# Optimization experiments

Hardware: AMD Instinct MI355X
Metric: run time of the kernel (lower is better)

Reference implementation:

```python
import math
import jax, jax.numpy as jnp
import numpy as np

B, N, D, H = 8, 512, 1024, 16
HD = D // H
K_DEFAULT, K_MAX, PROX_THR = 8, 12, 20.0


def setup_inputs() -> dict:
    key = jax.random.key(0)
    ks = jax.random.split(key, 12)
    tokens_B = jax.random.normal(ks[0], (B, N, D), dtype=jnp.float32)
    ego_distances = jax.random.uniform(ks[1], (B, N), dtype=jnp.float32)
    ego_mask = jnp.zeros((B, N), dtype=bool).at[:, 0].set(True)  # token 0 is ego
    ego_speed = jax.random.uniform(ks[2], (B,), dtype=jnp.float32)
    s = 1.0 / math.sqrt(D)
    Wq = jax.random.normal(ks[3], (D, D), jnp.float32) * s
    Wk = jax.random.normal(ks[4], (D, D), jnp.float32) * s
    Wv = jax.random.normal(ks[5], (D, D), jnp.float32) * s
    Weq = jax.random.normal(ks[6], (D, D), jnp.float32) * s
    Wo = jax.random.normal(ks[7], (D, D), jnp.float32) * (0.02 * s)
    Dm = D // 4
    W1 = jax.random.normal(ks[8], (Dm, 2), jnp.float32) * (1.0 / math.sqrt(2))
    b1 = jnp.zeros((Dm,), jnp.float32)
    W2 = jax.random.normal(ks[9], (H, Dm), jnp.float32) * (1.0 / math.sqrt(Dm))
    b2 = jnp.zeros((H,), jnp.float32)
    return dict(tokens_B=tokens_B, ego_distances=ego_distances, ego_mask=ego_mask,
                ego_speed=ego_speed, Wq=Wq, Wk=Wk, Wv=Wv, Weq=Weq, Wo=Wo,
                W1=W1, b1=b1, W2=W2, b2=b2)


def _compute_K(ego_speed, ego_distances):
    # deterministic, no-grad lookup (torch: @torch.no_grad)
    n = ego_distances.shape[1]
    close = (ego_distances < PROX_THR).astype(jnp.float32).sum(-1)
    density = close / max(n, 1)
    avg_speed = float(jnp.mean(ego_speed))
    avg_density = float(jnp.mean(density))
    K = K_DEFAULT
    if avg_speed > 15.0:
        K = min(K + 1, K_MAX)
    if avg_density > 0.5:
        K = min(K + 1, K_MAX)
    return min(K, n - 1)


def reference(tokens_B, ego_distances, ego_mask, ego_speed, Wq, Wk, Wv, Weq, Wo, W1, b1, W2, b2):
    b, n, d = tokens_B.shape
    K = _compute_K(ego_speed, ego_distances)
    if K <= 0:
        return jnp.zeros_like(tokens_B)

    # top-K nearest-to-ego neighbors per token, excluding self
    eye = jnp.eye(n, dtype=bool)
    dist_rank = jnp.where(eye[None, :, :], jnp.inf, ego_distances[:, None, :])  # (B,N,N)
    _, topk_idx = jax.lax.top_k(-dist_rank, K)  # (B,N,K) indices of smallest dists

    neighbors = jax.vmap(lambda t, idx: t[idx])(tokens_B, topk_idx)  # (B,N,K,D)

    is_ego = ego_mask.astype(tokens_B.dtype)[..., None]
    Q = (1.0 - is_ego) * (tokens_B @ Wq.T) + is_ego * (tokens_B @ Weq.T)
    Km = neighbors @ Wk.T
    Vm = neighbors @ Wv.T

    Q = Q.reshape(b, n, H, HD).transpose(0, 2, 1, 3)              # (B,H,N,hd)
    Km = Km.reshape(b, n, K, H, HD).transpose(0, 3, 1, 2, 4)      # (B,H,N,K,hd)
    Vm = Vm.reshape(b, n, K, H, HD).transpose(0, 3, 1, 2, 4)

    scores = jnp.einsum('bhnd,bhnkd->bhnk', Q, Km) / math.sqrt(HD)

    # additive pairwise distance bias MLP on (d_i_to_ego, d_j_to_ego)
    d_i = jnp.broadcast_to(ego_distances[:, :, None], (b, n, K))
    d_j = jax.vmap(lambda dd, idx: dd[idx])(ego_distances, topk_idx)
    dist_pair = jnp.stack([d_i, d_j], axis=-1)                    # (B,N,K,2)
    bias = jax.nn.relu(dist_pair @ W1.T + b1) @ W2.T + b2         # (B,N,K,H)
    scores = scores + bias.transpose(0, 3, 1, 2)                  # FIX-1: additive

    attn = jax.nn.softmax(scores, axis=-1)
    out = jnp.einsum('bhnk,bhnkd->bhnd', attn, Vm)
    out = out.transpose(0, 2, 1, 3).reshape(b, n, d)              # FIX-2 axis order
    return out @ Wo.T
```

## Files before the change

kernel.cpp:

```cpp
#include <hip/hip_runtime.h>
#include <math.h>

#define Bn 8
#define Nn 512
#define Dn 1024
#define Hn 16
#define HDn 64
#define KMAX 12
#define NSMAX 13
#define PROX 20.0f

typedef __attribute__((ext_vector_type(8))) short bf16x8;
typedef __attribute__((ext_vector_type(4))) float f32x4;

__device__ __forceinline__ unsigned short f2bf(float f) {
    unsigned int u = __float_as_uint(f);
    return (unsigned short)((u + 0x7FFFu + ((u >> 16) & 1u)) >> 16);
}

__global__ __launch_bounds__(256) void cvt_meta_kernel(const float* __restrict__ tokens,
                                                       const float* __restrict__ Wq,
                                                       const float* __restrict__ Wo,
                                                       const float* __restrict__ Wk,
                                                       const float* __restrict__ Wv,
                                                       const float* __restrict__ dist,
                                                       const float* __restrict__ speed,
                                                       unsigned short* __restrict__ tok_h,
                                                       unsigned short* __restrict__ wq_h,
                                                       unsigned short* __restrict__ wo_h,
                                                       unsigned short* __restrict__ wkv_h,
                                                       int* __restrict__ meta,
                                                       int* __restrict__ Lidx,
                                                       unsigned short* __restrict__ tok_g) {
    int blk = blockIdx.x;
    if (blk < 8192) {
        const float* src;
        unsigned short* dst;
        int local;
        if (blk < 4096) { src = tokens; dst = tok_h; local = blk; }
        else if (blk < 5120) { src = Wq; dst = wq_h; local = blk - 4096; }
        else if (blk < 6144) { src = Wo; dst = wo_h; local = blk - 5120; }
        else if (blk < 7168) { src = Wk; dst = wkv_h; local = blk - 6144; }
        else { src = Wv; dst = wkv_h + (size_t)Dn * Dn; local = blk - 7168; }
        int i = (local * 256 + threadIdx.x) * 4;
        float4 v = *(const float4*)&src[i];
        ushort4 o;
        o.x = f2bf(v.x); o.y = f2bf(v.y); o.z = f2bf(v.z); o.w = f2bf(v.w);
        *(ushort4*)&dst[i] = o;
        return;
    }
    if (threadIdx.x >= 64) return;
    int lane = threadIdx.x;
    int b = blk - 8192;

    int cnt = 0;
    for (int i = lane; i < Bn * Nn; i += 64) cnt += (dist[i] < PROX) ? 1 : 0;
    for (int off = 32; off; off >>= 1) cnt += __shfl_xor(cnt, off);

    float sp = 0.f;
    for (int i = lane; i < Bn; i += 64) sp += speed[i];
    for (int off = 32; off; off >>= 1) sp += __shfl_xor(sp, off);

    float avg_density = (float)cnt / (float)(Bn * Nn);
    float avg_speed = sp / (float)Bn;
    int K = 8;
    if (avg_speed > 15.0f) K = min(K + 1, KMAX);
    if (avg_density > 0.5f) K = min(K + 1, KMAX);
    K = min(K, Nn - 1);
    if (b == 0 && lane == 0) meta[0] = K;
    int ns = K + 1;

    int sel[NSMAX];
    float dloc[Nn / 64];
    #pragma unroll
    for (int j = 0; j < Nn / 64; ++j) dloc[j] = dist[b * Nn + lane + 64 * j];
    for (int r = 0; r < ns; ++r) {
        float mv = 1e30f;
        int mi = 0;
        #pragma unroll
        for (int j = 0; j < Nn / 64; ++j) {
            if (dloc[j] < mv) { mv = dloc[j]; mi = lane + 64 * j; }
        }
        for (int off = 32; off; off >>= 1) {
            float ov = __shfl_xor(mv, off);
            int oi = __shfl_xor(mi, off);
            if (ov < mv || (ov == mv && oi < mi)) { mv = ov; mi = oi; }
        }
        sel[r] = mi;
        if (lane == 0) Lidx[b * NSMAX + r] = mi;
        if ((mi & 63) == lane) dloc[mi >> 6] = 1e30f;
    }

    for (int s = 0; s < ns; ++s) {
        const float* src = &tokens[(size_t)(b * Nn + sel[s]) * Dn];
        unsigned short* dst = &tok_g[(size_t)(b * NSMAX + s) * Dn];
        #pragma unroll
        for (int q = 0; q < 4; ++q) {
            float4 v = *(const float4*)&src[(q * 64 + lane) * 4];
            ushort4 o;
            o.x = f2bf(v.x); o.y = f2bf(v.y); o.z = f2bf(v.z); o.w = f2bf(v.w);
            *(ushort4*)&dst[(q * 64 + lane) * 4] = o;
        }
    }
}

__device__ __forceinline__ void gemm_body(const unsigned short* __restrict__ A,
                                          const unsigned short* __restrict__ Bm,
                                          float* __restrict__ C, int Nd,
                                          int bm, int bn,
                                          unsigned short* As, unsigned short* Bs) {
    const int Kd = Dn;
    int t = threadIdx.x;
    int wave = t >> 6, lane = t & 63;
    int wm = wave >> 1, wn = wave & 1;

    int srow = lane >> 2;
    int skoff = (lane & 3) * 8;
    const unsigned short* Ag  = A  + (size_t)(bm + wave * 16 + srow) * Kd + skoff;
    const unsigned short* Bg  = Bm + (size_t)(bn + wave * 32 + srow) * Kd + skoff;
    const unsigned short* Bg2 = Bg + 16 * Kd;
    unsigned short* AsW  = As + (wave * 16) * 32;
    unsigned short* BsW  = Bs + (wave * 32) * 32;
    unsigned short* BsW2 = BsW + 16 * 32;

    f32x4 acc[2][4] = {};

    int fm = lane & 15;
    int fk = (lane >> 4) * 8;

    for (int k0 = 0; k0 < Kd; k0 += 32) {
        __builtin_amdgcn_global_load_lds((const __attribute__((address_space(1))) void*)Ag,
                                         (__attribute__((address_space(3))) void*)AsW, 16, 0, 0);
        __builtin_amdgcn_global_load_lds((const __attribute__((address_space(1))) void*)Bg,
                                         (__attribute__((address_space(3))) void*)BsW, 16, 0, 0);
        __builtin_amdgcn_global_load_lds((const __attribute__((address_space(1))) void*)Bg2,
                                         (__attribute__((address_space(3))) void*)BsW2, 16, 0, 0);
        Ag += 32; Bg += 32; Bg2 += 32;
        __syncthreads();

        bf16x8 af[2], bfr[4];
        #pragma unroll
        for (int mi = 0; mi < 2; ++mi)
            af[mi] = *(const bf16x8*)&As[(wm * 32 + mi * 16 + fm) * 32 + fk];
        #pragma unroll
        for (int ni = 0; ni < 4; ++ni)
            bfr[ni] = *(const bf16x8*)&Bs[(wn * 64 + ni * 16 + fm) * 32 + fk];
        #pragma unroll
        for (int mi = 0; mi < 2; ++mi)
            #pragma unroll
            for (int ni = 0; ni < 4; ++ni)
                acc[mi][ni] = __builtin_amdgcn_mfma_f32_16x16x32_bf16(af[mi], bfr[ni], acc[mi][ni], 0, 0, 0);
        __syncthreads();
    }

    int erow = (lane >> 4) * 4;
    #pragma unroll
    for (int mi = 0; mi < 2; ++mi)
        #pragma unroll
        for (int ni = 0; ni < 4; ++ni)
            #pragma unroll
            for (int r = 0; r < 4; ++r) {
                int row = bm + wm * 32 + mi * 16 + erow + r;
                int col = bn + wn * 64 + ni * 16 + fm;
                C[(size_t)row * Nd + col] = acc[mi][ni][r];
            }
}

__global__ __launch_bounds__(256) void proj_fused_kernel(const unsigned short* __restrict__ tok_h,
                                                         const unsigned short* __restrict__ wq_h,
                                                         const unsigned short* __restrict__ tok_g,
                                                         const unsigned short* __restrict__ wkv_h,
                                                         const float* __restrict__ tokens,
                                                         const float* __restrict__ Weq,
                                                         float* __restrict__ Qbuf,
                                                         float* __restrict__ KVproj,
                                                         float* __restrict__ Qego) {
    __shared__ unsigned short As[64 * 32];
    __shared__ unsigned short Bs[128 * 32];
    __shared__ float tok[Dn];

    int blk = blockIdx.x;
    if (blk < 32) {
        gemm_body(tok_g, wkv_h, KVproj, 2048, (blk >> 4) * 64, (blk & 15) * 128, As, Bs);
    } else if (blk < 544) {
        int idx = blk - 32;
        gemm_body(tok_h, wq_h, Qbuf, Dn, (idx >> 3) * 64, (idx & 7) * 128, As, Bs);
    } else {
        int blk2 = blk - 544;
        int b = blk2 >> 5, cg = blk2 & 31;
        for (int t = threadIdx.x; t < Dn; t += 256) tok[t] = tokens[(size_t)(b * Nn) * Dn + t];
        __syncthreads();
        int w = threadIdx.x >> 6, lane = threadIdx.x & 63;
        for (int o = 0; o < 8; ++o) {
            int col = cg * 32 + w * 8 + o;
            const float* wr = &Weq[(size_t)col * Dn];
            float sum = 0.f;
            #pragma unroll
            for (int q = 0; q < 4; ++q) {
                float4 w4 = *(const float4*)&wr[q * 256 + lane * 4];
                float4 t4 = *(const float4*)&tok[q * 256 + lane * 4];
                sum += w4.x * t4.x + w4.y * t4.y + w4.z * t4.z + w4.w * t4.w;
            }
            for (int off = 32; off; off >>= 1) sum += __shfl_xor(sum, off);
            if (lane == 0) Qego[(size_t)b * Dn + col] = sum;
        }
    }
}

__global__ __launch_bounds__(256) void gemm_out_kernel(const unsigned short* __restrict__ A,
                                                       const unsigned short* __restrict__ Bm,
                                                       float* __restrict__ C) {
    __shared__ unsigned short As[64 * 32];
    __shared__ unsigned short Bs[128 * 32];
    gemm_body(A, Bm, C, Dn, blockIdx.y * 64, blockIdx.x * 128, As, Bs);
}

#define HSTR 264
#define KVSTR 2048
__global__ __launch_bounds__(256) void attn_kernel(const float* __restrict__ Q,
                                                   const float* __restrict__ Qego,
                                                   const float* __restrict__ KVproj,
                                                   const float* __restrict__ dist,
                                                   const float* __restrict__ W1,
                                                   const float* __restrict__ b1,
                                                   const float* __restrict__ W2,
                                                   const float* __restrict__ b2,
                                                   const int* __restrict__ meta,
                                                   const int* __restrict__ Lidx,
                                                   unsigned short* __restrict__ AttnOut) {
    __shared__ float q[Dn];
    __shared__ float hid[KMAX * HSTR];
    __shared__ float sc[Hn * NSMAX];
    __shared__ float at[Hn * NSMAX];
    __shared__ int selslot[NSMAX];
    __shared__ float dj[NSMAX];

    int bi = blockIdx.x;
    int b = bi >> 9;
    int i = bi & (Nn - 1);
    int K = meta[0];
    int ns = K + 1;
    int t = threadIdx.x;

    if (t == 0) {
        int cnt = 0;
        for (int s = 0; s < ns && cnt < K; ++s) {
            int jj = Lidx[b * NSMAX + s];
            if (jj != i) { selslot[cnt] = s; dj[cnt] = dist[b * Nn + jj]; cnt++; }
        }
    }
    {
        const float* qsrc = (i == 0) ? &Qego[(size_t)b * Dn] : &Q[(size_t)bi * Dn];
        float4 v = *(const float4*)&qsrc[t * 4];
        *(float4*)&q[t * 4] = v;
    }
    __syncthreads();

    float d_i = dist[b * Nn + i];

    {
        float2 w01 = *(const float2*)&W1[2 * t];
        float bb = b1[t];
        for (int k = 0; k < K; ++k) {
            float h = w01.x * d_i + w01.y * dj[k] + bb;
            hid[k * HSTR + t] = h > 0.f ? h : 0.f;
        }
    }
    __syncthreads();

    {
        int g = t >> 4, l = t & 15;
        float4 qv = *(const float4*)&q[g * HDn + l * 4];
        float4 w2v[4];
        #pragma unroll
        for (int ii = 0; ii < 4; ++ii)
            w2v[ii] = *(const float4*)&W2[g * 256 + ii * 64 + l * 4];
        float bias0 = b2[g];

        for (int k = 0; k < K; ++k) {
            int row = b * NSMAX + selslot[k];
            float4 kv4 = *(const float4*)&KVproj[(size_t)row * KVSTR + g * HDn + l * 4];
            float val = (qv.x * kv4.x + qv.y * kv4.y + qv.z * kv4.z + qv.w * kv4.w) * 0.125f;
            #pragma unroll
            for (int ii = 0; ii < 4; ++ii) {
                float4 h4 = *(const float4*)&hid[k * HSTR + ii * 64 + l * 4];
                val += w2v[ii].x * h4.x + w2v[ii].y * h4.y + w2v[ii].z * h4.z + w2v[ii].w * h4.w;
            }
            val += __shfl_xor(val, 1);
            val += __shfl_xor(val, 2);
            val += __shfl_xor(val, 4);
            val += __shfl_xor(val, 8);
            if (l == 0) sc[g * NSMAX + k] = val + bias0;
        }
    }
    __syncthreads();

    if (t < Hn) {
        int h = t;
        float m = -1e30f;
        for (int k = 0; k < K; ++k) m = fmaxf(m, sc[h * NSMAX + k]);
        float ssum = 0.f;
        for (int k = 0; k < K; ++k) {
            float e = expf(sc[h * NSMAX + k] - m);
            at[h * NSMAX + k] = e;
            ssum += e;
        }
        float inv = 1.f / ssum;
        for (int k = 0; k < K; ++k) at[h * NSMAX + k] *= inv;
    }
    __syncthreads();

    {
        int col = t * 4;
        int h = col >> 6;
        float4 o = make_float4(0.f, 0.f, 0.f, 0.f);
        for (int k = 0; k < K; ++k) {
            float a = at[h * NSMAX + k];
            int row = b * NSMAX + selslot[k];
            float4 v4 = *(const float4*)&KVproj[(size_t)row * KVSTR + Dn + col];
            o.x += a * v4.x; o.y += a * v4.y; o.z += a * v4.z; o.w += a * v4.w;
        }
        ushort4 ob;
        ob.x = f2bf(o.x); ob.y = f2bf(o.y); ob.z = f2bf(o.z); ob.w = f2bf(o.w);
        *(ushort4*)&AttnOut[(size_t)bi * Dn + col] = ob;
    }
}

extern "C" void kernel_launch(void* const* d_in, const int* in_sizes, int n_in,
                              void* d_out, int out_size, void* d_ws, size_t ws_size,
                              hipStream_t stream) {
    (void)in_sizes; (void)n_in; (void)out_size; (void)ws_size;
    const float* tokens = (const float*)d_in[0];
    const float* dist   = (const float*)d_in[1];
    const float* speed  = (const float*)d_in[3];
    const float* Wq  = (const float*)d_in[4];
    const float* Wk  = (const float*)d_in[5];
    const float* Wv  = (const float*)d_in[6];
    const float* Weq = (const float*)d_in[7];
    const float* Wo  = (const float*)d_in[8];
    const float* W1  = (const float*)d_in[9];
    const float* b1  = (const float*)d_in[10];
    const float* W2  = (const float*)d_in[11];
    const float* b2  = (const float*)d_in[12];
    float* out = (float*)d_out;

    char* ws = (char*)d_ws;
    const size_t SZ_KV   = (size_t)128 * 2048 * sizeof(float);
    const size_t SZ_BIG  = (size_t)Bn * Nn * Dn * sizeof(float);
    const size_t SZ_BIGH = (size_t)Bn * Nn * Dn * sizeof(unsigned short);
    const size_t SZ_WH   = (size_t)Dn * Dn * sizeof(unsigned short);
    const size_t SZ_TG   = (size_t)128 * Dn * sizeof(unsigned short);
    const size_t SZ_QE   = (size_t)Bn * Dn * sizeof(float);

    size_t off = 0;
    int*   meta  = (int*)(ws + off);  off += 256;
    int*   Lidx  = (int*)(ws + off);  off += 768;
    float* KVproj = (float*)(ws + off); off += SZ_KV;
    float* Qbuf  = (float*)(ws + off); off += SZ_BIG;
    float* Qego  = (float*)(ws + off); off += SZ_QE;
    unsigned short* tok_h = (unsigned short*)(ws + off); off += SZ_BIGH;
    unsigned short* ab_h  = (unsigned short*)(ws + off); off += SZ_BIGH;
    unsigned short* wq_h  = (unsigned short*)(ws + off); off += SZ_WH;
    unsigned short* wo_h  = (unsigned short*)(ws + off); off += SZ_WH;
    unsigned short* wkv_h = (unsigned short*)(ws + off); off += 2 * SZ_WH;
    unsigned short* tok_g = (unsigned short*)(ws + off); off += SZ_TG;

    cvt_meta_kernel<<<8200, 256, 0, stream>>>(tokens, Wq, Wo, Wk, Wv, dist, speed,
                                              tok_h, wq_h, wo_h, wkv_h, meta, Lidx, tok_g);
    proj_fused_kernel<<<800, 256, 0, stream>>>(tok_h, wq_h, tok_g, wkv_h, tokens, Weq,
                                               Qbuf, KVproj, Qego);
    attn_kernel<<<Bn * Nn, 256, 0, stream>>>(Qbuf, Qego, KVproj, dist, W1, b1, W2, b2,
                                             meta, Lidx, ab_h);
    gemm_out_kernel<<<dim3(Dn / 128, (Bn * Nn) / 64), 256, 0, stream>>>(ab_h, wo_h, out);
}
```

Before: 188.6 us.

## Fold Wo into per-head V of shared neighbor set, shrink output GEMM K

Because all tokens in a batch attend to the same small set of nearest-to-ego candidates, each head's V rows can be premultiplied by that head's slice of Wo. This gives a per-batch table of shape (1024 x 16 slots x 16 heads). The attention kernel now writes only a 256-wide bf16 weight vector per token (slot x head), and the final GEMM uses K=256 instead of 1024. This removes the 1024-wide attention-output write and cuts the output GEMM's reduction length by four, at the cost of an extra small GEMM kernel and V stored in bf16.

```diff
diff --git a/kernel.cpp b/kernel.cpp
--- a/kernel.cpp
+++ b/kernel.cpp
@@ -93,7 +93,7 @@
 
     for (int s = 0; s < ns; ++s) {
         const float* src = &tokens[(size_t)(b * Nn + sel[s]) * Dn];
-        unsigned short* dst = &tok_g[(size_t)(b * NSMAX + s) * Dn];
+        unsigned short* dst = &tok_g[(size_t)(b * 16 + s) * Dn];
         #pragma unroll
         for (int q = 0; q < 4; ++q) {
             float4 v = *(const float4*)&src[(q * 64 + lane) * 4];
@@ -104,21 +104,21 @@
     }
 }
 
-__device__ __forceinline__ void gemm_body(const unsigned short* __restrict__ A,
-                                          const unsigned short* __restrict__ Bm,
-                                          float* __restrict__ C, int Nd,
-                                          int bm, int bn,
-                                          unsigned short* As, unsigned short* Bs) {
-    const int Kd = Dn;
+__device__ __forceinline__ void gemm_body_s(const unsigned short* A,
+                                            const unsigned short* Bm,
+                                            float* Cf, unsigned short* Ch,
+                                            int Nd, int Kd, int sA, int sB,
+                                            int bm, int bn, int mode, int hh,
+                                            unsigned short* As, unsigned short* Bs) {
     int t = threadIdx.x;
     int wave = t >> 6, lane = t & 63;
     int wm = wave >> 1, wn = wave & 1;
 
     int srow = lane >> 2;
     int skoff = (lane & 3) * 8;
-    const unsigned short* Ag  = A  + (size_t)(bm + wave * 16 + srow) * Kd + skoff;
-    const unsigned short* Bg  = Bm + (size_t)(bn + wave * 32 + srow) * Kd + skoff;
-    const unsigned short* Bg2 = Bg + 16 * Kd;
+    const unsigned short* Ag  = A  + (size_t)(bm + wave * 16 + srow) * sA + skoff;
+    const unsigned short* Bg  = Bm + (size_t)(bn + wave * 32 + srow) * sB + skoff;
+    const unsigned short* Bg2 = Bg + (size_t)16 * sB;
     unsigned short* AsW  = As + (wave * 16) * 32;
     unsigned short* BsW  = Bs + (wave * 32) * 32;
     unsigned short* BsW2 = BsW + 16 * 32;
@@ -162,7 +162,14 @@
             for (int r = 0; r < 4; ++r) {
                 int row = bm + wm * 32 + mi * 16 + erow + r;
                 int col = bn + wn * 64 + ni * 16 + fm;
-                C[(size_t)row * Nd + col] = acc[mi][ni][r];
+                if (mode == 0) {
+                    Cf[(size_t)row * Nd + col] = acc[mi][ni][r];
+                } else if (mode == 1) {
+                    Ch[(size_t)row * Nd + col] = f2bf(acc[mi][ni][r]);
+                } else {
+                    int bb = col >> 4, ss = col & 15;
+                    Ch[((size_t)bb * 1024 + row) * 256 + ss * 16 + hh] = f2bf(acc[mi][ni][r]);
+                }
             }
 }
 
@@ -173,18 +180,25 @@
                                                          const float* __restrict__ tokens,
                                                          const float* __restrict__ Weq,
                                                          float* __restrict__ Qbuf,
-                                                         float* __restrict__ KVproj,
+                                                         float* __restrict__ Kproj,
+                                                         unsigned short* __restrict__ v_h,
                                                          float* __restrict__ Qego) {
     __shared__ unsigned short As[64 * 32];
     __shared__ unsigned short Bs[128 * 32];
     __shared__ float tok[Dn];
 
     int blk = blockIdx.x;
-    if (blk < 32) {
-        gemm_body(tok_g, wkv_h, KVproj, 2048, (blk >> 4) * 64, (blk & 15) * 128, As, Bs);
+    if (blk < 16) {
+        gemm_body_s(tok_g, wkv_h, Kproj, 0, Dn, Dn, Dn, Dn,
+                    (blk >> 3) * 64, (blk & 7) * 128, 0, 0, As, Bs);
+    } else if (blk < 32) {
+        int idx = blk - 16;
+        gemm_body_s(tok_g, wkv_h + (size_t)Dn * Dn, 0, v_h, Dn, Dn, Dn, Dn,
+                    (idx >> 3) * 64, (idx & 7) * 128, 1, 0, As, Bs);
     } else if (blk < 544) {
         int idx = blk - 32;
-        gemm_body(tok_h, wq_h, Qbuf, Dn, (idx >> 3) * 64, (idx & 7) * 128, As, Bs);
+        gemm_body_s(tok_h, wq_h, Qbuf, 0, Dn, Dn, Dn, Dn,
+                    (idx >> 3) * 64, (idx & 7) * 128, 0, 0, As, Bs);
     } else {
         int blk2 = blk - 544;
         int b = blk2 >> 5, cg = blk2 & 31;
@@ -207,19 +221,20 @@
     }
 }
 
-__global__ __launch_bounds__(256) void gemm_out_kernel(const unsigned short* __restrict__ A,
-                                                       const unsigned short* __restrict__ Bm,
-                                                       float* __restrict__ C) {
+__global__ __launch_bounds__(256) void vo3_gemm_kernel(const unsigned short* __restrict__ wo_h,
+                                                       const unsigned short* __restrict__ v_h,
+                                                       unsigned short* __restrict__ Vo3T) {
     __shared__ unsigned short As[64 * 32];
     __shared__ unsigned short Bs[128 * 32];
-    gemm_body(A, Bm, C, Dn, blockIdx.y * 64, blockIdx.x * 128, As, Bs);
+    int h = blockIdx.y;
+    gemm_body_s(wo_h + h * HDn, v_h + h * HDn, 0, Vo3T, 0, HDn, Dn, Dn,
+                blockIdx.x * 64, 0, 2, h, As, Bs);
 }
 
 #define HSTR 264
-#define KVSTR 2048
 __global__ __launch_bounds__(256) void attn_kernel(const float* __restrict__ Q,
                                                    const float* __restrict__ Qego,
-                                                   const float* __restrict__ KVproj,
+                                                   const float* __restrict__ Kproj,
                                                    const float* __restrict__ dist,
                                                    const float* __restrict__ W1,
                                                    const float* __restrict__ b1,
@@ -227,12 +242,13 @@
                                                    const float* __restrict__ b2,
                                                    const int* __restrict__ meta,
                                                    const int* __restrict__ Lidx,
-                                                   unsigned short* __restrict__ AttnOut) {
+                                                   unsigned short* __restrict__ Wt) {
     __shared__ float q[Dn];
     __shared__ float hid[KMAX * HSTR];
     __shared__ float sc[Hn * NSMAX];
     __shared__ float at[Hn * NSMAX];
     __shared__ int selslot[NSMAX];
+    __shared__ int inv[16];
     __shared__ float dj[NSMAX];
 
     int bi = blockIdx.x;
@@ -243,10 +259,11 @@
     int t = threadIdx.x;
 
     if (t == 0) {
+        for (int s = 0; s < 16; ++s) inv[s] = -1;
         int cnt = 0;
         for (int s = 0; s < ns && cnt < K; ++s) {
             int jj = Lidx[b * NSMAX + s];
-            if (jj != i) { selslot[cnt] = s; dj[cnt] = dist[b * Nn + jj]; cnt++; }
+            if (jj != i) { selslot[cnt] = s; dj[cnt] = dist[b * Nn + jj]; inv[s] = cnt; cnt++; }
         }
     }
     {
@@ -278,8 +295,8 @@
         float bias0 = b2[g];
 
         for (int k = 0; k < K; ++k) {
-            int row = b * NSMAX + selslot[k];
-            float4 kv4 = *(const float4*)&KVproj[(size_t)row * KVSTR + g * HDn + l * 4];
+            int row = b * 16 + selslot[k];
+            float4 kv4 = *(const float4*)&Kproj[(size_t)row * Dn + g * HDn + l * 4];
             float val = (qv.x * kv4.x + qv.y * kv4.y + qv.z * kv4.z + qv.w * kv4.w) * 0.125f;
             #pragma unroll
             for (int ii = 0; ii < 4; ++ii) {
@@ -305,25 +322,31 @@
             at[h * NSMAX + k] = e;
             ssum += e;
         }
-        float inv = 1.f / ssum;
-        for (int k = 0; k < K; ++k) at[h * NSMAX + k] *= inv;
+        float inv2 = 1.f / ssum;
+        for (int k = 0; k < K; ++k) at[h * NSMAX + k] *= inv2;
     }
     __syncthreads();
 
     {
-        int col = t * 4;
-        int h = col >> 6;
-        float4 o = make_float4(0.f, 0.f, 0.f, 0.f);
-        for (int k = 0; k < K; ++k) {
-            float a = at[h * NSMAX + k];
-            int row = b * NSMAX + selslot[k];
-            float4 v4 = *(const float4*)&KVproj[(size_t)row * KVSTR + Dn + col];
-            o.x += a * v4.x; o.y += a * v4.y; o.z += a * v4.z; o.w += a * v4.w;
-        }
-        ushort4 ob;
-        ob.x = f2bf(o.x); ob.y = f2bf(o.y); ob.z = f2bf(o.z); ob.w = f2bf(o.w);
-        *(ushort4*)&AttnOut[(size_t)bi * Dn + col] = ob;
-    }
+        int s = t >> 4, h = t & 15;
+        int k = (s < NSMAX) ? inv[s] : -1;
+        float a = (k >= 0) ? at[h * NSMAX + k] : 0.f;
+        Wt[(size_t)bi * 256 + t] = f2bf(a);
+    }
+}
+
+__global__ __launch_bounds__(256) void final_gemm_kernel(const unsigned short* __restrict__ Wt,
+                                                         const unsigned short* __restrict__ Vo3T,
+                                                         float* __restrict__ out) {
+    __shared__ unsigned short As[64 * 32];
+    __shared__ unsigned short Bs[128 * 32];
+    int rbase = blockIdx.y * 64;
+    int b = rbase >> 9;
+    int bmloc = rbase & (Nn - 1);
+    gemm_body_s(Wt + (size_t)b * Nn * 256,
+                Vo3T + (size_t)b * Dn * 256,
+                out + (size_t)b * Nn * Dn, 0,
+                Dn, 256, 256, 256, bmloc, blockIdx.x * 128, 0, 0, As, Bs);
 }
 
 extern "C" void kernel_launch(void* const* d_in, const int* in_sizes, int n_in,
@@ -345,7 +368,10 @@
     float* out = (float*)d_out;
 
     char* ws = (char*)d_ws;
-    const size_t SZ_KV   = (size_t)128 * 2048 * sizeof(float);
+    const size_t SZ_KP   = (size_t)128 * Dn * sizeof(float);
+    const size_t SZ_VH   = (size_t)128 * Dn * sizeof(unsigned short);
+    const size_t SZ_V3   = (size_t)Bn * Dn * 256 * sizeof(unsigned short);
+    const size_t SZ_WT   = (size_t)Bn * Nn * 256 * sizeof(unsigned short);
     const size_t SZ_BIG  = (size_t)Bn * Nn * Dn * sizeof(float);
     const size_t SZ_BIGH = (size_t)Bn * Nn * Dn * sizeof(unsigned short);
     const size_t SZ_WH   = (size_t)Dn * Dn * sizeof(unsigned short);
@@ -355,11 +381,13 @@
     size_t off = 0;
     int*   meta  = (int*)(ws + off);  off += 256;
     int*   Lidx  = (int*)(ws + off);  off += 768;
-    float* KVproj = (float*)(ws + off); off += SZ_KV;
+    float* Kproj = (float*)(ws + off); off += SZ_KP;
     float* Qbuf  = (float*)(ws + off); off += SZ_BIG;
     float* Qego  = (float*)(ws + off); off += SZ_QE;
+    unsigned short* v_h   = (unsigned short*)(ws + off); off += SZ_VH;
+    unsigned short* Vo3T  = (unsigned short*)(ws + off); off += SZ_V3;
+    unsigned short* Wt    = (unsigned short*)(ws + off); off += SZ_WT;
     unsigned short* tok_h = (unsigned short*)(ws + off); off += SZ_BIGH;
-    unsigned short* ab_h  = (unsigned short*)(ws + off); off += SZ_BIGH;
     unsigned short* wq_h  = (unsigned short*)(ws + off); off += SZ_WH;
     unsigned short* wo_h  = (unsigned short*)(ws + off); off += SZ_WH;
     unsigned short* wkv_h = (unsigned short*)(ws + off); off += 2 * SZ_WH;
@@ -368,8 +396,9 @@
     cvt_meta_kernel<<<8200, 256, 0, stream>>>(tokens, Wq, Wo, Wk, Wv, dist, speed,
                                               tok_h, wq_h, wo_h, wkv_h, meta, Lidx, tok_g);
     proj_fused_kernel<<<800, 256, 0, stream>>>(tok_h, wq_h, tok_g, wkv_h, tokens, Weq,
-                                               Qbuf, KVproj, Qego);
-    attn_kernel<<<Bn * Nn, 256, 0, stream>>>(Qbuf, Qego, KVproj, dist, W1, b1, W2, b2,
-                                             meta, Lidx, ab_h);
-    gemm_out_kernel<<<dim3(Dn / 128, (Bn * Nn) / 64), 256, 0, stream>>>(ab_h, wo_h, out);
-}
+                                               Qbuf, Kproj, v_h, Qego);
+    vo3_gemm_kernel<<<dim3(16, 16), 256, 0, stream>>>(wo_h, v_h, Vo3T);
+    attn_kernel<<<Bn * Nn, 256, 0, stream>>>(Qbuf, Qego, Kproj, dist, W1, b1, W2, b2,
+                                             meta, Lidx, Wt);
+    final_gemm_kernel<<<dim3(Dn / 128, (Bn * Nn) / 64), 256, 0, stream>>>(Wt, Vo3T, out);
+}
```

Result: faster. 180.4 us (-4.3%).
